# Optimization experiments

Hardware: AMD Instinct MI355X
Metric: run time of the kernel (lower is better)

Reference implementation:

```python
import jax, jax.numpy as jnp
import numpy as np

B, T, C, H = 2, 2048, 1024, 16
D = C // H  # head_dim = 64

def setup_inputs() -> dict:
    key = jax.random.key(0)
    ks = jax.random.split(key, 9)
    s = 1.0 / np.sqrt(C)
    return {
        "x": jax.random.normal(ks[0], (B, T, C), dtype=jnp.float32),
        "Wq": jax.random.uniform(ks[1], (C, C), jnp.float32, -s, s),
        "bq": jax.random.uniform(ks[2], (C,), jnp.float32, -s, s),
        "Wk": jax.random.uniform(ks[3], (C, C), jnp.float32, -s, s),
        "bk": jax.random.uniform(ks[4], (C,), jnp.float32, -s, s),
        "Wv": jax.random.uniform(ks[5], (C, C), jnp.float32, -s, s),
        "bv": jax.random.uniform(ks[6], (C,), jnp.float32, -s, s),
        "Wp": jax.random.uniform(ks[7], (C, C), jnp.float32, -s, s),
        "bp": jax.random.uniform(ks[8], (C,), jnp.float32, -s, s),
    }

def reference(x, Wq, bq, Wk, bk, Wv, bv, Wp, bp):
    # Linear layers: torch nn.Linear weight is [out,in], so x @ W.T + b
    q = x @ Wq.T + bq
    k = x @ Wk.T + bk
    v = x @ Wv.T + bv
    # [B,T,C] -> [B,H,T,D]
    q = q.reshape(B, T, H, D).transpose(0, 2, 1, 3)
    k = k.reshape(B, T, H, D).transpose(0, 2, 1, 3)
    v = v.reshape(B, T, H, D).transpose(0, 2, 1, 3)
    att = jnp.einsum("bhqd,bhkd->bhqk", q, k) / jnp.sqrt(jnp.float32(D))
    causal = jnp.tril(jnp.ones((T, T), dtype=bool))  # [T,T]
    att = jnp.where(causal, att, jnp.float32(-jnp.inf))
    att = jax.nn.softmax(att, axis=-1)
    out = jnp.einsum("bhqk,bhkd->bhqd", att, v)
    out = out.transpose(0, 2, 1, 3).reshape(B, T, C)
    return out @ Wp.T + bp
```

## Files before the change

### kernel.cpp

```cpp
#include <hip/hip_runtime.h>
#include <hip/hip_bf16.h>

typedef __bf16 bf16x8 __attribute__((ext_vector_type(8)));
typedef __bf16 bf16x4 __attribute__((ext_vector_type(4)));
typedef __bf16 bf16x2 __attribute__((ext_vector_type(2)));
typedef float  f32x4  __attribute__((ext_vector_type(4)));
typedef float  f32x16v __attribute__((ext_vector_type(16)));

#define MFMA16(A,B,Cc) __builtin_amdgcn_mfma_f32_16x16x32_bf16(A,B,Cc,0,0,0)
#define MFMA32(A,B,Cc) __builtin_amdgcn_mfma_f32_32x32x16_bf16(A,B,Cc,0,0,0)

__device__ inline unsigned pack2(float a, float b) {
  union { bf16x2 v; unsigned u; } t;
  t.v[0] = (__bf16)a; t.v[1] = (__bf16)b;
  return t.u;
}
__device__ inline bf16x8 frag4(unsigned w0, unsigned w1, unsigned w2, unsigned w3) {
  union { unsigned u[4]; bf16x8 v; } t;
  t.u[0] = w0; t.u[1] = w1; t.u[2] = w2; t.u[3] = w3;
  return t.v;
}

__global__ __launch_bounds__(256) void conv_kernel(
    const float* __restrict__ x,
    const float* __restrict__ Wq, const float* __restrict__ Wk,
    const float* __restrict__ Wv, const float* __restrict__ Wp,
    __bf16* __restrict__ xb, __bf16* __restrict__ Wb)
{
  const int z = blockIdx.y;
  const float* src;
  __bf16* dst;
  int n4;
  if (z == 0) { src = x;  dst = xb; n4 = 1048576; }
  else {
    src = (z == 1) ? Wq : (z == 2) ? Wk : (z == 3) ? Wv : Wp;
    dst = Wb + (size_t)(z - 1) * 1048576;
    n4  = 262144;
  }
  const f32x4* s4 = (const f32x4*)src;
  for (int i = blockIdx.x * 256 + threadIdx.x; i < n4; i += gridDim.x * 256) {
    const f32x4 v = s4[i];
    bf16x4 o;
#pragma unroll
    for (int j = 0; j < 4; ++j) o[j] = (__bf16)v[j];
    *(bf16x4*)(dst + (size_t)i * 4) = o;
  }
}

__device__ inline void gemm_core(const __bf16* __restrict__ A,
                                 const __bf16* __restrict__ W,
                                 int m0, int n0,
                                 __bf16* As, __bf16* Bs,
                                 f32x4 (&acc)[4][4])
{
  const int tid = threadIdx.x, lane = tid & 63;
  const int wid = tid >> 6, wr = wid >> 1, wc = wid & 1;
  const int g = lane >> 4, cl = lane & 15;
  const int sr = tid >> 2, sk = (tid & 3) * 8;

  for (int k0 = 0; k0 < 1024; k0 += 32) {
    bf16x8 a0 = *(const bf16x8*)(A + (size_t)(m0 + sr)      * 1024 + k0 + sk);
    bf16x8 a1 = *(const bf16x8*)(A + (size_t)(m0 + sr + 64) * 1024 + k0 + sk);
    bf16x8 b0 = *(const bf16x8*)(W + (size_t)(n0 + sr)      * 1024 + k0 + sk);
    bf16x8 b1 = *(const bf16x8*)(W + (size_t)(n0 + sr + 64) * 1024 + k0 + sk);
    __syncthreads();
    *(bf16x8*)(As + sr * 32 + sk)        = a0;
    *(bf16x8*)(As + (sr + 64) * 32 + sk) = a1;
    *(bf16x8*)(Bs + sr * 32 + sk)        = b0;
    *(bf16x8*)(Bs + (sr + 64) * 32 + sk) = b1;
    __syncthreads();
    bf16x8 af[4], bfr[4];
#pragma unroll
    for (int m = 0; m < 4; ++m)
      af[m] = *(const bf16x8*)(As + (wr * 64 + m * 16 + cl) * 32 + g * 8);
#pragma unroll
    for (int n = 0; n < 4; ++n)
      bfr[n] = *(const bf16x8*)(Bs + (wc * 64 + n * 16 + cl) * 32 + g * 8);
#pragma unroll
    for (int m = 0; m < 4; ++m)
#pragma unroll
      for (int n = 0; n < 4; ++n)
        acc[m][n] = MFMA16(af[m], bfr[n], acc[m][n]);
  }
}

__global__ __launch_bounds__(256) void gemm_qkv128(
    const __bf16* __restrict__ xb, const __bf16* __restrict__ Wb,
    const float* __restrict__ bq, const float* __restrict__ bk,
    const float* __restrict__ bv,
    __bf16* __restrict__ Qw, __bf16* __restrict__ Kw, __bf16* __restrict__ Vw)
{
  __shared__ __align__(16) __bf16 As[128 * 32];
  __shared__ __align__(16) __bf16 Bs[128 * 32];

  const int orig = blockIdx.x;
  const int wg   = (orig & 7) * 96 + (orig >> 3);
  const int z    = wg >> 8;
  const int rem  = wg & 255;
  const int m0   = (rem >> 3) * 128;
  const int n0   = (rem & 7) * 128;

  const __bf16* W  = Wb + (size_t)z * 1048576;
  const float*  bi = (z == 0) ? bq : (z == 1) ? bk : bv;
  __bf16*       out = (z == 0) ? Qw : (z == 1) ? Kw : Vw;

  f32x4 acc[4][4] = {};
  gemm_core(xb, W, m0, n0, As, Bs, acc);

  const int lane = threadIdx.x & 63, wid = threadIdx.x >> 6;
  const int wr = wid >> 1, wc = wid & 1;
  const int g = lane >> 4, cl = lane & 15;

  float bvv[4];
#pragma unroll
  for (int n = 0; n < 4; ++n) bvv[n] = bi[n0 + wc * 64 + n * 16 + cl];

#pragma unroll
  for (int m = 0; m < 4; ++m)
#pragma unroll
    for (int n = 0; n < 4; ++n) {
      const int col = n0 + wc * 64 + n * 16 + cl;
      const int h = col >> 6, d = col & 63;
      if (z == 2) {
        const int row0 = m0 + wr * 64 + m * 16 + g * 4;
        const int b2 = row0 >> 11, t0 = row0 & 2047;
        bf16x4 v4;
#pragma unroll
        for (int j = 0; j < 4; ++j) v4[j] = (__bf16)(acc[m][n][j] + bvv[n]);
        *(bf16x4*)(out + (size_t)(b2 * 16 + h) * 131072 + (size_t)d * 2048 + t0) = v4;
      } else {
#pragma unroll
        for (int j = 0; j < 4; ++j) {
          const int row = m0 + wr * 64 + m * 16 + g * 4 + j;
          const int b2 = row >> 11, t = row & 2047;
          out[(size_t)(b2 * 16 + h) * 131072 + (size_t)t * 64 + d] =
              (__bf16)(acc[m][n][j] + bvv[n]);
        }
      }
    }
}

__global__ __launch_bounds__(256) void gemm_proj128(
    const __bf16* __restrict__ A, const __bf16* __restrict__ W,
    const float* __restrict__ bi, float* __restrict__ outp)
{
  __shared__ __align__(16) __bf16 As[128 * 32];
  __shared__ __align__(16) __bf16 Bs[128 * 32];

  const int orig = blockIdx.x;
  const int wg   = (orig & 7) * 32 + (orig >> 3);
  const int m0   = (wg >> 3) * 128;
  const int n0   = (wg & 7) * 128;

  f32x4 acc[4][4] = {};
  gemm_core(A, W, m0, n0, As, Bs, acc);

  const int lane = threadIdx.x & 63, wid = threadIdx.x >> 6;
  const int wr = wid >> 1, wc = wid & 1;
  const int g = lane >> 4, cl = lane & 15;

  float bvv[4];
#pragma unroll
  for (int n = 0; n < 4; ++n) bvv[n] = bi[n0 + wc * 64 + n * 16 + cl];
#pragma unroll
  for (int m = 0; m < 4; ++m)
#pragma unroll
    for (int n = 0; n < 4; ++n) {
      const int col = n0 + wc * 64 + n * 16 + cl;
#pragma unroll
      for (int j = 0; j < 4; ++j) {
        const int row = m0 + wr * 64 + m * 16 + g * 4 + j;
        outp[(size_t)row * 1024 + col] = acc[m][n][j] + bvv[n];
      }
    }
}

__global__ __launch_bounds__(128, 4) void attn_kernel(
    const __bf16* __restrict__ Q, const __bf16* __restrict__ K,
    const __bf16* __restrict__ Vt, __bf16* __restrict__ Oc)
{
  const int bh    = blockIdx.x;
  const int strip = 63 - (int)blockIdx.y;
  const int wid   = threadIdx.x >> 6;
  const int lane  = threadIdx.x & 63;
  const int l31 = lane & 31, hi = lane >> 5;
  const int qs = strip * 32;

  const __bf16* Qb = Q  + (size_t)bh * 131072;
  const __bf16* Kb = K  + (size_t)bh * 131072;
  const __bf16* Vb = Vt + (size_t)bh * 131072;

  const int ntiles = strip + 1;
  const int nA   = (ntiles + 1) >> 1;
  const int tBeg = wid ? nA : 0;
  const int tEnd = wid ? ntiles : nA;

  bf16x8 qf[4];
#pragma unroll
  for (int c = 0; c < 4; ++c)
    qf[c] = *(const bf16x8*)(Qb + (qs + l31) * 64 + c * 16 + hi * 8);

  f32x16v o0 = {}, o1 = {};
  float M = -1e30f, L = 0.f;
  const float SC = 0.18033688f;

  const __bf16* vrow0 = Vb + (size_t)l31 * 2048;
  const __bf16* vrow1 = Vb + (size_t)(32 + l31) * 2048;

  for (int t = tBeg; t < tEnd; ++t) {
    const int kv0 = t * 32;
    f32x16v s = {};
#pragma unroll
    for (int c = 0; c < 4; ++c) {
      bf16x8 kf = *(const bf16x8*)(Kb + (kv0 + l31) * 64 + c * 16 + hi * 8);
      s = MFMA32(kf, qf[c], s);
    }
    float sv[16];
#pragma unroll
    for (int r = 0; r < 16; ++r) sv[r] = s[r];
    if (t == ntiles - 1) {
#pragma unroll
      for (int r = 0; r < 16; ++r) {
        const int kl = (r & 3) + 8 * (r >> 2) + 4 * hi;
        if (kl > l31) sv[r] = -1e30f;
      }
    }
    float mt = sv[0];
#pragma unroll
    for (int r = 1; r < 16; ++r) mt = fmaxf(mt, sv[r]);
    mt = fmaxf(mt, __shfl_xor(mt, 32, 64));
    if (!__all(mt <= M)) {
      const float Mn = fmaxf(M, mt);
      const float rs = exp2f((M - Mn) * SC);
      o0 *= rs; o1 *= rs; L *= rs; M = Mn;
    }
    float p[16];
    float lt = 0.f;
#pragma unroll
    for (int r = 0; r < 16; ++r) { p[r] = exp2f((sv[r] - M) * SC); lt += p[r]; }
    lt += __shfl_xor(lt, 32, 64);
    L += lt;

    const unsigned c0 = pack2(p[0],  p[1]),  c1 = pack2(p[2],  p[3]);
    const unsigned c2 = pack2(p[4],  p[5]),  c3 = pack2(p[6],  p[7]);
    const unsigned c4 = pack2(p[8],  p[9]),  c5 = pack2(p[10], p[11]);
    const unsigned c6 = pack2(p[12], p[13]), c7 = pack2(p[14], p[15]);
    const unsigned x0 = __shfl_xor(c0, 32, 64), x1 = __shfl_xor(c1, 32, 64);
    const unsigned x2 = __shfl_xor(c2, 32, 64), x3 = __shfl_xor(c3, 32, 64);
    const unsigned x4 = __shfl_xor(c4, 32, 64), x5 = __shfl_xor(c5, 32, 64);
    const unsigned x6 = __shfl_xor(c6, 32, 64), x7 = __shfl_xor(c7, 32, 64);
    const bf16x8 pf0 = frag4(hi ? x2 : c0, hi ? x3 : c1, hi ? c2 : x0, hi ? c3 : x1);
    const bf16x8 pf1 = frag4(hi ? x6 : c4, hi ? x7 : c5, hi ? c6 : x4, hi ? c7 : x5);

    bf16x8 va;
    va = *(const bf16x8*)(vrow0 + kv0 + hi * 8);       o0 = MFMA32(va, pf0, o0);
    va = *(const bf16x8*)(vrow0 + kv0 + 16 + hi * 8);  o0 = MFMA32(va, pf1, o0);
    va = *(const bf16x8*)(vrow1 + kv0 + hi * 8);       o1 = MFMA32(va, pf0, o1);
    va = *(const bf16x8*)(vrow1 + kv0 + 16 + hi * 8);  o1 = MFMA32(va, pf1, o1);
  }

  __shared__ float Sm[64][34];
  if (wid == 1) {
#pragma unroll
    for (int q4 = 0; q4 < 4; ++q4) {
      f32x4 a = { o0[q4*4+0], o0[q4*4+1], o0[q4*4+2], o0[q4*4+3] };
      f32x4 b = { o1[q4*4+0], o1[q4*4+1], o1[q4*4+2], o1[q4*4+3] };
      *(f32x4*)&Sm[lane][q4 * 4]      = a;
      *(f32x4*)&Sm[lane][16 + q4 * 4] = b;
    }
    Sm[lane][32] = M;
    Sm[lane][33] = L;
  }
  __syncthreads();
  if (wid == 0) {
    const float M1 = Sm[lane][32];
    const float L1 = Sm[lane][33];
    const float Ms = fmaxf(M, M1);
    const float r0 = exp2f((M  - Ms) * SC);
    const float r1 = exp2f((M1 - Ms) * SC);
    const float inv = 1.0f / (L * r0 + L1 * r1);

    const int b = bh >> 4, h = bh & 15;
    const int tq = qs + l31;
    __bf16* orow = Oc + (size_t)(b * 2048 + tq) * 1024 + h * 64;
#pragma unroll
    for (int q4 = 0; q4 < 4; ++q4) {
      bf16x4 v0, v1;
#pragma unroll
      for (int j = 0; j < 4; ++j) {
        const int r = q4 * 4 + j;
        v0[j] = (__bf16)((o0[r] * r0 + Sm[lane][r]      * r1) * inv);
        v1[j] = (__bf16)((o1[r] * r0 + Sm[lane][16 + r] * r1) * inv);
      }
      const int d0 = 8 * q4 + 4 * hi;
      *(bf16x4*)(orow + d0)      = v0;
      *(bf16x4*)(orow + 32 + d0) = v1;
    }
  }
}

extern "C" void kernel_launch(void* const* d_in, const int* in_sizes, int n_in,
                              void* d_out, int out_size, void* d_ws, size_t ws_size,
                              hipStream_t stream) {
  const float* x  = (const float*)d_in[0];
  const float* Wq = (const float*)d_in[1];
  const float* bq = (const float*)d_in[2];
  const float* Wk = (const float*)d_in[3];
  const float* bk = (const float*)d_in[4];
  const float* Wv = (const float*)d_in[5];
  const float* bv = (const float*)d_in[6];
  const float* Wp = (const float*)d_in[7];
  const float* bp = (const float*)d_in[8];

  __bf16* Qw  = (__bf16*)d_ws;
  __bf16* Kw  = Qw + (size_t)4194304;
  __bf16* Vw  = Kw + (size_t)4194304;
  __bf16* xbA = Vw + (size_t)4194304;
  __bf16* Wb  = xbA + (size_t)4194304;

  conv_kernel<<<dim3(512, 5), 256, 0, stream>>>(x, Wq, Wk, Wv, Wp, xbA, Wb);
  gemm_qkv128<<<768, 256, 0, stream>>>(xbA, Wb, bq, bk, bv, Qw, Kw, Vw);
  attn_kernel<<<dim3(32, 64), 128, 0, stream>>>(Qw, Kw, Vw, xbA );
  gemm_proj128<<<256, 256, 0, stream>>>(xbA , Wb + (size_t)3 * 1048576,
                                        bp, (float*)d_out);
}
```

Baseline: 145.4 us.

## Split attention KV range across four waves with lazy rescale threshold

The attention block grows from two to four waves, each handling a quarter of the causal KV tiles, and the combine step merges three partial results through shared memory. Online-softmax rescaling is skipped unless the running max grows by more than a threshold, and the exponent argument is folded into one fma with a precomputed scaled max. The goal is more parallelism per query strip and fewer rescale operations, at the cost of a larger combine and more shared memory. Deferring the rescale lets exponents exceed 1, which relies on the values staying within float range.

```diff
diff --git a/kernel.cpp b/kernel.cpp
--- a/kernel.cpp
+++ b/kernel.cpp
@@ -175,7 +175,7 @@
     }
 }
 
-__global__ __launch_bounds__(128, 4) void attn_kernel(
+__global__ __launch_bounds__(256, 6) void attn_kernel(
     const __bf16* __restrict__ Q, const __bf16* __restrict__ K,
     const __bf16* __restrict__ Vt, __bf16* __restrict__ Oc)
 {
@@ -191,9 +191,8 @@
   const __bf16* Vb = Vt + (size_t)bh * 131072;
 
   const int ntiles = strip + 1;
-  const int nA   = (ntiles + 1) >> 1;
-  const int tBeg = wid ? nA : 0;
-  const int tEnd = wid ? ntiles : nA;
+  const int tBeg = (wid * ntiles) >> 2;
+  const int tEnd = ((wid + 1) * ntiles) >> 2;
 
   bf16x8 qf[4];
 #pragma unroll
@@ -203,6 +202,8 @@
   f32x16v o0 = {}, o1 = {};
   float M = -1e30f, L = 0.f;
   const float SC = 0.18033688f;
+  const float DT = 16.6f;
+  float MS = M * SC;
 
   const __bf16* vrow0 = Vb + (size_t)l31 * 2048;
   const __bf16* vrow1 = Vb + (size_t)(32 + l31) * 2048;
@@ -229,15 +230,18 @@
 #pragma unroll
     for (int r = 1; r < 16; ++r) mt = fmaxf(mt, sv[r]);
     mt = fmaxf(mt, __shfl_xor(mt, 32, 64));
-    if (!__all(mt <= M)) {
+    if (!__all(mt <= M + DT)) {
       const float Mn = fmaxf(M, mt);
       const float rs = exp2f((M - Mn) * SC);
-      o0 *= rs; o1 *= rs; L *= rs; M = Mn;
+      o0 *= rs; o1 *= rs; L *= rs; M = Mn; MS = M * SC;
     }
     float p[16];
     float lt = 0.f;
 #pragma unroll
-    for (int r = 0; r < 16; ++r) { p[r] = exp2f((sv[r] - M) * SC); lt += p[r]; }
+    for (int r = 0; r < 16; ++r) {
+      p[r] = exp2f(__builtin_fmaf(sv[r], SC, -MS));
+      lt += p[r];
+    }
     lt += __shfl_xor(lt, 32, 64);
     L += lt;
 
@@ -259,26 +263,37 @@
     va = *(const bf16x8*)(vrow1 + kv0 + 16 + hi * 8);  o1 = MFMA32(va, pf1, o1);
   }
 
-  __shared__ float Sm[64][34];
-  if (wid == 1) {
+  __shared__ float Sm[3][64][35];
+  if (wid != 0) {
+    float* dst = &Sm[wid - 1][lane][0];
 #pragma unroll
     for (int q4 = 0; q4 < 4; ++q4) {
       f32x4 a = { o0[q4*4+0], o0[q4*4+1], o0[q4*4+2], o0[q4*4+3] };
       f32x4 b = { o1[q4*4+0], o1[q4*4+1], o1[q4*4+2], o1[q4*4+3] };
-      *(f32x4*)&Sm[lane][q4 * 4]      = a;
-      *(f32x4*)&Sm[lane][16 + q4 * 4] = b;
-    }
-    Sm[lane][32] = M;
-    Sm[lane][33] = L;
+      *(f32x4*)(dst + q4 * 4)      = a;
+      *(f32x4*)(dst + 16 + q4 * 4) = b;
+    }
+    dst[32] = M;
+    dst[33] = L;
   }
   __syncthreads();
   if (wid == 0) {
-    const float M1 = Sm[lane][32];
-    const float L1 = Sm[lane][33];
-    const float Ms = fmaxf(M, M1);
-    const float r0 = exp2f((M  - Ms) * SC);
-    const float r1 = exp2f((M1 - Ms) * SC);
-    const float inv = 1.0f / (L * r0 + L1 * r1);
+    float Mw[3], Lw[3];
+#pragma unroll
+    for (int w = 0; w < 3; ++w) {
+      Mw[w] = Sm[w][lane][32];
+      Lw[w] = Sm[w][lane][33];
+    }
+    float Ms = fmaxf(fmaxf(M, Mw[0]), fmaxf(Mw[1], Mw[2]));
+    const float r0 = exp2f((M - Ms) * SC);
+    float rw[3];
+    float Lt = L * r0;
+#pragma unroll
+    for (int w = 0; w < 3; ++w) {
+      rw[w] = exp2f((Mw[w] - Ms) * SC);
+      Lt += Lw[w] * rw[w];
+    }
+    const float inv = 1.0f / Lt;
 
     const int b = bh >> 4, h = bh & 15;
     const int tq = qs + l31;
@@ -289,8 +304,15 @@
 #pragma unroll
       for (int j = 0; j < 4; ++j) {
         const int r = q4 * 4 + j;
-        v0[j] = (__bf16)((o0[r] * r0 + Sm[lane][r]      * r1) * inv);
-        v1[j] = (__bf16)((o1[r] * r0 + Sm[lane][16 + r] * r1) * inv);
+        float a = o0[r] * r0;
+        float bb2 = o1[r] * r0;
+#pragma unroll
+        for (int w = 0; w < 3; ++w) {
+          a   += Sm[w][lane][r]      * rw[w];
+          bb2 += Sm[w][lane][16 + r] * rw[w];
+        }
+        v0[j] = (__bf16)(a * inv);
+        v1[j] = (__bf16)(bb2 * inv);
       }
       const int d0 = 8 * q4 + 4 * hi;
       *(bf16x4*)(orow + d0)      = v0;
@@ -320,7 +342,7 @@
 
   conv_kernel<<<dim3(512, 5), 256, 0, stream>>>(x, Wq, Wk, Wv, Wp, xbA, Wb);
   gemm_qkv128<<<768, 256, 0, stream>>>(xbA, Wb, bq, bk, bv, Qw, Kw, Vw);
-  attn_kernel<<<dim3(32, 64), 128, 0, stream>>>(Qw, Kw, Vw, xbA );
+  attn_kernel<<<dim3(32, 64), 256, 0, stream>>>(Qw, Kw, Vw, xbA );
   gemm_proj128<<<256, 256, 0, stream>>>(xbA , Wb + (size_t)3 * 1048576,
                                         bp, (float*)d_out);
 }
```

New measurement: 184.9 us. 1.27x slower.

## Process two KV tiles per attention iteration with lazy max rescaling

Applied to the files above, without the earlier changes.

The attention inner loop now handles two 32-key tiles per iteration, issuing both QK^T MFMA chains together to expose more independent work and amortize the max/sum reductions and the shuffles. Rescaling of the running output is skipped unless the new row max exceeds the old one by a threshold, and the exponent is computed with a single FMA against a precomputed scaled max. Tree reductions replace the linear max and sum chains. The lazy rescale lets unnormalized exponentials grow by up to about 2^3, which is safe in fp32 but adds numeric slack. The unrolled body also uses more registers.

```diff
diff --git a/kernel.cpp b/kernel.cpp
--- a/kernel.cpp
+++ b/kernel.cpp
@@ -19,6 +19,21 @@
   union { unsigned u[4]; bf16x8 v; } t;
   t.u[0] = w0; t.u[1] = w1; t.u[2] = w2; t.u[3] = w3;
   return t.v;
+}
+__device__ inline float hmax16(const f32x16v& v) {
+  float a = fmaxf(v[0], v[1]),  b = fmaxf(v[2], v[3]);
+  float c = fmaxf(v[4], v[5]),  d = fmaxf(v[6], v[7]);
+  float e = fmaxf(v[8], v[9]),  f = fmaxf(v[10], v[11]);
+  float g = fmaxf(v[12], v[13]), h = fmaxf(v[14], v[15]);
+  return fmaxf(fmaxf(fmaxf(a, b), fmaxf(c, d)),
+               fmaxf(fmaxf(e, f), fmaxf(g, h)));
+}
+__device__ inline float hsum16(const f32x16v& v) {
+  float a = v[0] + v[1],  b = v[2] + v[3];
+  float c = v[4] + v[5],  d = v[6] + v[7];
+  float e = v[8] + v[9],  f = v[10] + v[11];
+  float g = v[12] + v[13], h = v[14] + v[15];
+  return ((a + b) + (c + d)) + ((e + f) + (g + h));
 }
 
 __global__ __launch_bounds__(256) void conv_kernel(
@@ -203,60 +218,122 @@
   f32x16v o0 = {}, o1 = {};
   float M = -1e30f, L = 0.f;
   const float SC = 0.18033688f;
+  const float DT = 16.6f;
+  float MS = M * SC;
 
   const __bf16* vrow0 = Vb + (size_t)l31 * 2048;
   const __bf16* vrow1 = Vb + (size_t)(32 + l31) * 2048;
 
-  for (int t = tBeg; t < tEnd; ++t) {
+  int t = tBeg;
+  for (; t + 2 <= tEnd; t += 2) {
+    const int kv0 = t * 32, kv1 = kv0 + 32;
+    f32x16v sa = {}, sb = {};
+#pragma unroll
+    for (int c = 0; c < 4; ++c) {
+      bf16x8 kfa = *(const bf16x8*)(Kb + (kv0 + l31) * 64 + c * 16 + hi * 8);
+      bf16x8 kfb = *(const bf16x8*)(Kb + (kv1 + l31) * 64 + c * 16 + hi * 8);
+      sa = MFMA32(kfa, qf[c], sa);
+      sb = MFMA32(kfb, qf[c], sb);
+    }
+    if (t + 1 == ntiles - 1) {
+#pragma unroll
+      for (int r = 0; r < 16; ++r) {
+        const int kl = (r & 3) + 8 * (r >> 2) + 4 * hi;
+        if (kl > l31) sb[r] = -1e30f;
+      }
+    }
+    float mt = fmaxf(hmax16(sa), hmax16(sb));
+    mt = fmaxf(mt, __shfl_xor(mt, 32, 64));
+    if (!__all(mt <= M + DT)) {
+      const float Mn = fmaxf(M, mt);
+      const float rs = exp2f((M - Mn) * SC);
+      o0 *= rs; o1 *= rs; L *= rs; M = Mn; MS = M * SC;
+    }
+#pragma unroll
+    for (int r = 0; r < 16; ++r) {
+      sa[r] = exp2f(__builtin_fmaf(sa[r], SC, -MS));
+      sb[r] = exp2f(__builtin_fmaf(sb[r], SC, -MS));
+    }
+    float lt = hsum16(sa) + hsum16(sb);
+    lt += __shfl_xor(lt, 32, 64);
+    L += lt;
+
+    const unsigned a0 = pack2(sa[0],  sa[1]),  a1 = pack2(sa[2],  sa[3]);
+    const unsigned a2 = pack2(sa[4],  sa[5]),  a3 = pack2(sa[6],  sa[7]);
+    const unsigned a4 = pack2(sa[8],  sa[9]),  a5 = pack2(sa[10], sa[11]);
+    const unsigned a6 = pack2(sa[12], sa[13]), a7 = pack2(sa[14], sa[15]);
+    const unsigned b0 = pack2(sb[0],  sb[1]),  b1 = pack2(sb[2],  sb[3]);
+    const unsigned b2 = pack2(sb[4],  sb[5]),  b3 = pack2(sb[6],  sb[7]);
+    const unsigned b4 = pack2(sb[8],  sb[9]),  b5 = pack2(sb[10], sb[11]);
+    const unsigned b6 = pack2(sb[12], sb[13]), b7 = pack2(sb[14], sb[15]);
+    const unsigned xa0 = __shfl_xor(a0, 32, 64), xa1 = __shfl_xor(a1, 32, 64);
+    const unsigned xa2 = __shfl_xor(a2, 32, 64), xa3 = __shfl_xor(a3, 32, 64);
+    const unsigned xa4 = __shfl_xor(a4, 32, 64), xa5 = __shfl_xor(a5, 32, 64);
+    const unsigned xa6 = __shfl_xor(a6, 32, 64), xa7 = __shfl_xor(a7, 32, 64);
+    const unsigned xb0 = __shfl_xor(b0, 32, 64), xb1 = __shfl_xor(b1, 32, 64);
+    const unsigned xb2 = __shfl_xor(b2, 32, 64), xb3 = __shfl_xor(b3, 32, 64);
+    const unsigned xb4 = __shfl_xor(b4, 32, 64), xb5 = __shfl_xor(b5, 32, 64);
+    const unsigned xb6 = __shfl_xor(b6, 32, 64), xb7 = __shfl_xor(b7, 32, 64);
+    const bf16x8 pf0a = frag4(hi ? xa2 : a0, hi ? xa3 : a1, hi ? a2 : xa0, hi ? a3 : xa1);
+    const bf16x8 pf1a = frag4(hi ? xa6 : a4, hi ? xa7 : a5, hi ? a6 : xa4, hi ? a7 : xa5);
+    const bf16x8 pf0b = frag4(hi ? xb2 : b0, hi ? xb3 : b1, hi ? b2 : xb0, hi ? b3 : xb1);
+    const bf16x8 pf1b = frag4(hi ? xb6 : b4, hi ? xb7 : b5, hi ? b6 : xb4, hi ? b7 : xb5);
+
+    bf16x8 va;
+    va = *(const bf16x8*)(vrow0 + kv0 + hi * 8);       o0 = MFMA32(va, pf0a, o0);
+    va = *(const bf16x8*)(vrow1 + kv0 + hi * 8);       o1 = MFMA32(va, pf0a, o1);
+    va = *(const bf16x8*)(vrow0 + kv0 + 16 + hi * 8);  o0 = MFMA32(va, pf1a, o0);
+    va = *(const bf16x8*)(vrow1 + kv0 + 16 + hi * 8);  o1 = MFMA32(va, pf1a, o1);
+    va = *(const bf16x8*)(vrow0 + kv1 + hi * 8);       o0 = MFMA32(va, pf0b, o0);
+    va = *(const bf16x8*)(vrow1 + kv1 + hi * 8);       o1 = MFMA32(va, pf0b, o1);
+    va = *(const bf16x8*)(vrow0 + kv1 + 16 + hi * 8);  o0 = MFMA32(va, pf1b, o0);
+    va = *(const bf16x8*)(vrow1 + kv1 + 16 + hi * 8);  o1 = MFMA32(va, pf1b, o1);
+  }
+  if (t < tEnd) {
     const int kv0 = t * 32;
-    f32x16v s = {};
+    f32x16v sa = {};
 #pragma unroll
     for (int c = 0; c < 4; ++c) {
       bf16x8 kf = *(const bf16x8*)(Kb + (kv0 + l31) * 64 + c * 16 + hi * 8);
-      s = MFMA32(kf, qf[c], s);
-    }
-    float sv[16];
-#pragma unroll
-    for (int r = 0; r < 16; ++r) sv[r] = s[r];
+      sa = MFMA32(kf, qf[c], sa);
+    }
     if (t == ntiles - 1) {
 #pragma unroll
       for (int r = 0; r < 16; ++r) {
         const int kl = (r & 3) + 8 * (r >> 2) + 4 * hi;
-        if (kl > l31) sv[r] = -1e30f;
+        if (kl > l31) sa[r] = -1e30f;
       }
     }
-    float mt = sv[0];
-#pragma unroll
-    for (int r = 1; r < 16; ++r) mt = fmaxf(mt, sv[r]);
+    float mt = hmax16(sa);
     mt = fmaxf(mt, __shfl_xor(mt, 32, 64));
-    if (!__all(mt <= M)) {
+    if (!__all(mt <= M + DT)) {
       const float Mn = fmaxf(M, mt);
       const float rs = exp2f((M - Mn) * SC);
-      o0 *= rs; o1 *= rs; L *= rs; M = Mn;
-    }
-    float p[16];
-    float lt = 0.f;
-#pragma unroll
-    for (int r = 0; r < 16; ++r) { p[r] = exp2f((sv[r] - M) * SC); lt += p[r]; }
+      o0 *= rs; o1 *= rs; L *= rs; M = Mn; MS = M * SC;
+    }
+#pragma unroll
+    for (int r = 0; r < 16; ++r)
+      sa[r] = exp2f(__builtin_fmaf(sa[r], SC, -MS));
+    float lt = hsum16(sa);
     lt += __shfl_xor(lt, 32, 64);
     L += lt;
 
-    const unsigned c0 = pack2(p[0],  p[1]),  c1 = pack2(p[2],  p[3]);
-    const unsigned c2 = pack2(p[4],  p[5]),  c3 = pack2(p[6],  p[7]);
-    const unsigned c4 = pack2(p[8],  p[9]),  c5 = pack2(p[10], p[11]);
-    const unsigned c6 = pack2(p[12], p[13]), c7 = pack2(p[14], p[15]);
-    const unsigned x0 = __shfl_xor(c0, 32, 64), x1 = __shfl_xor(c1, 32, 64);
-    const unsigned x2 = __shfl_xor(c2, 32, 64), x3 = __shfl_xor(c3, 32, 64);
-    const unsigned x4 = __shfl_xor(c4, 32, 64), x5 = __shfl_xor(c5, 32, 64);
-    const unsigned x6 = __shfl_xor(c6, 32, 64), x7 = __shfl_xor(c7, 32, 64);
-    const bf16x8 pf0 = frag4(hi ? x2 : c0, hi ? x3 : c1, hi ? c2 : x0, hi ? c3 : x1);
-    const bf16x8 pf1 = frag4(hi ? x6 : c4, hi ? x7 : c5, hi ? c6 : x4, hi ? c7 : x5);
+    const unsigned a0 = pack2(sa[0],  sa[1]),  a1 = pack2(sa[2],  sa[3]);
+    const unsigned a2 = pack2(sa[4],  sa[5]),  a3 = pack2(sa[6],  sa[7]);
+    const unsigned a4 = pack2(sa[8],  sa[9]),  a5 = pack2(sa[10], sa[11]);
+    const unsigned a6 = pack2(sa[12], sa[13]), a7 = pack2(sa[14], sa[15]);
+    const unsigned xa0 = __shfl_xor(a0, 32, 64), xa1 = __shfl_xor(a1, 32, 64);
+    const unsigned xa2 = __shfl_xor(a2, 32, 64), xa3 = __shfl_xor(a3, 32, 64);
+    const unsigned xa4 = __shfl_xor(a4, 32, 64), xa5 = __shfl_xor(a5, 32, 64);
+    const unsigned xa6 = __shfl_xor(a6, 32, 64), xa7 = __shfl_xor(a7, 32, 64);
+    const bf16x8 pf0a = frag4(hi ? xa2 : a0, hi ? xa3 : a1, hi ? a2 : xa0, hi ? a3 : xa1);
+    const bf16x8 pf1a = frag4(hi ? xa6 : a4, hi ? xa7 : a5, hi ? a6 : xa4, hi ? a7 : xa5);
 
     bf16x8 va;
-    va = *(const bf16x8*)(vrow0 + kv0 + hi * 8);       o0 = MFMA32(va, pf0, o0);
-    va = *(const bf16x8*)(vrow0 + kv0 + 16 + hi * 8);  o0 = MFMA32(va, pf1, o0);
-    va = *(const bf16x8*)(vrow1 + kv0 + hi * 8);       o1 = MFMA32(va, pf0, o1);
-    va = *(const bf16x8*)(vrow1 + kv0 + 16 + hi * 8);  o1 = MFMA32(va, pf1, o1);
+    va = *(const bf16x8*)(vrow0 + kv0 + hi * 8);       o0 = MFMA32(va, pf0a, o0);
+    va = *(const bf16x8*)(vrow1 + kv0 + hi * 8);       o1 = MFMA32(va, pf0a, o1);
+    va = *(const bf16x8*)(vrow0 + kv0 + 16 + hi * 8);  o0 = MFMA32(va, pf1a, o0);
+    va = *(const bf16x8*)(vrow1 + kv0 + 16 + hi * 8);  o1 = MFMA32(va, pf1a, o1);
   }
 
   __shared__ float Sm[64][34];
```

Result: slower. 149.6 us (+2.9%).
